# Optimization experiments

Hardware: AMD Instinct MI355X
Metric: run time of the kernel (lower is better)

Reference implementation:

```python
import jax, jax.numpy as jnp
import numpy as np

N = 100000        # nodes
E = 1600000       # edges
DES, TWEET, NUMP, CATP = 768, 768, 6, 11
IN_DIM, H, R = 512, 128, 2
BR = IN_DIM // 4  # per-branch width = 128


def setup_inputs() -> dict:
    key = jax.random.key(0)
    ks = jax.random.split(key, 16)
    w = lambda k, s: jax.random.normal(k, s, jnp.float32) * 0.02
    z = lambda d: jnp.zeros((d,), jnp.float32)
    return {
        "x": jax.random.normal(ks[0], (N, NUMP + TWEET + CATP + DES), jnp.float32),
        "edge_index": jax.random.randint(ks[1], (2, E), 0, N),
        "edge_type": jax.random.randint(ks[2], (E,), 0, R),
        "W_des": w(ks[3], (DES, BR)),   "b_des": z(BR),
        "W_tweet": w(ks[4], (TWEET, BR)), "b_tweet": z(BR),
        "W_num": w(ks[5], (NUMP, BR)),  "b_num": z(BR),
        "W_cat": w(ks[6], (CATP, BR)),  "b_cat": z(BR),
        "W_in": w(ks[7], (IN_DIM, H)),  "b_in": z(H),
        "prelu_a": jnp.full((H,), 0.25, jnp.float32),
        "root1": w(ks[8], (H, H)), "rel1": w(ks[9], (R, H, H)), "bias1": z(H),
        "root2": w(ks[10], (H, H)), "rel2": w(ks[11], (R, H, H)), "bias2": z(H),
        "W_cls": w(ks[12], (H, H)), "b_cls": z(H),
    }


def _leaky(v):
    return jnp.where(v >= 0, v, 0.01 * v)


def _rgcn(h, src, dst, edge_type, root, rel_w, bias):
    # PyG RGCNConv (default mean aggregation per relation):
    # out_i = bias + h_i @ root + sum_r mean_{j in N_r(i)} h_j @ W_r
    out = h @ root + bias
    for r in range(R):  # R is small and fixed
        mask = (edge_type == r).astype(h.dtype)          # [E]
        msg = (h @ rel_w[r])[src] * mask[:, None]        # [E, H]
        agg = jax.ops.segment_sum(msg, dst, num_segments=N)
        cnt = jax.ops.segment_sum(mask, dst, num_segments=N)
        out = out + agg / jnp.maximum(cnt, 1.0)[:, None]
    return out


def reference(x, edge_index, edge_type,
              W_des, b_des, W_tweet, b_tweet, W_num, b_num, W_cat, b_cat,
              W_in, b_in, prelu_a,
              root1, rel1, bias1, root2, rel2, bias2, W_cls, b_cls):
    # feature column layout: [num_prop | tweet | cat_prop | des]
    num_prop = x[:, :NUMP]
    tweet = x[:, NUMP:NUMP + TWEET]
    cat_prop = x[:, NUMP + TWEET:NUMP + TWEET + CATP]
    des = x[:, NUMP + TWEET + CATP:]

    d = _leaky(des @ W_des + b_des)
    t = _leaky(tweet @ W_tweet + b_tweet)
    n = _leaky(num_prop @ W_num + b_num)
    c = _leaky(cat_prop @ W_cat + b_cat)
    h = jnp.concatenate((d, t, n, c), axis=1) @ W_in + b_in
    h = jnp.where(h >= 0, h, prelu_a * h)  # PReLU, per-channel alpha

    src, dst = edge_index[0], edge_index[1]
    h = _rgcn(h, src, dst, edge_type, root1, rel1, bias1)
    h = _rgcn(h, src, dst, edge_type, root2, rel2, bias2)
    return h @ W_cls + b_cls
```

## Files before the change

kernel.cpp:

```cpp
#include <hip/hip_runtime.h>
#include <cstdint>
#include <cstddef>

#define NN 100000
#define EE 1600000
#define XDIM 1553
#define HD 128

typedef __attribute__((ext_vector_type(8))) short short8;
typedef __attribute__((ext_vector_type(4))) float f32x4;
typedef float f32x4u __attribute__((vector_size(16), aligned(4)));

union Frag { unsigned int u[4]; short8 s; uint4 v; };

#define OFF_DES_HI 0
#define OFF_DES_LO 98304
#define OFF_TW_HI  196608
#define OFF_TW_LO  294912
#define OFF_NUM_HI 393216
#define OFF_NUM_LO 397312
#define OFF_CAT_HI 401408
#define OFF_CAT_LO 405504
#define OFF_WIN_HI 409600
#define OFF_WIN_LO 475136
#define OFF_L1_HI  540672
#define OFF_L1_LO  589824
#define OFF_L2_HI  638976
#define OFF_L2_LO  688128
#define OFF_CLS_HI 737280
#define OFF_CLS_LO 753664
#define WT_SITES   385024

#define PREPW_BLOCKS 1504
#define COUNT_BLOCKS 6250
#define PROJ_NBLK    1563
#define FILL_BLOCKS  6250

__device__ __forceinline__ void cvt_pair(float f0, float f1,
                                         unsigned int& hi, unsigned int& lo) {
  unsigned int u0 = __float_as_uint(f0), u1 = __float_as_uint(f1);
  hi = __builtin_amdgcn_perm(u1, u0, 0x07060302u);
  float l0 = f0 - __uint_as_float(u0 & 0xFFFF0000u);
  float l1 = f1 - __uint_as_float(u1 & 0xFFFF0000u);
  lo = __builtin_amdgcn_perm(__float_as_uint(l1), __float_as_uint(l0), 0x07060302u);
}

__device__ __forceinline__ unsigned short bf16_rne(float f) {
  unsigned int u = __float_as_uint(f);
  return (unsigned short)((u + 0x7FFFu + ((u >> 16) & 1u)) >> 16);
}

__device__ __forceinline__ void fence_barrier() {
  asm volatile("" ::: "memory");
  __builtin_amdgcn_s_barrier();
  asm volatile("" ::: "memory");
}
__device__ __forceinline__ void lgkm0_barrier() {
  asm volatile("s_waitcnt lgkmcnt(0)" ::: "memory");
  __builtin_amdgcn_s_barrier();
  asm volatile("" ::: "memory");
}

__global__ __launch_bounds__(256) void k_setup(
    const float* __restrict__ Wdes, const float* __restrict__ Wtw,
    const float* __restrict__ Wnum, const float* __restrict__ Wcat,
    const float* __restrict__ Win,  const float* __restrict__ root1,
    const float* __restrict__ rel1, const float* __restrict__ root2,
    const float* __restrict__ rel2, const float* __restrict__ Wcls,
    unsigned short* __restrict__ Wt,
    const int* __restrict__ ei, const int* __restrict__ et,
    int* __restrict__ cnt2) {
  if (blockIdx.x >= PREPW_BLOCKS) {
    int e = (blockIdx.x - PREPW_BLOCKS) * 256 + threadIdx.x;
    if (e < EE) atomicAdd(&cnt2[et[e] * NN + ei[EE + e]], 1);
    return;
  }
  int id = blockIdx.x * 256 + threadIdx.x;
  if (id >= WT_SITES) return;
  const float* src; int K, Kpad, dhi, dlo, local;
  if (id < 98304)       { src=Wdes;        K=768; Kpad=768; dhi=OFF_DES_HI;       dlo=OFF_DES_LO;       local=id; }
  else if (id < 196608) { src=Wtw;         K=768; Kpad=768; dhi=OFF_TW_HI;        dlo=OFF_TW_LO;        local=id-98304; }
  else if (id < 200704) { src=Wnum;        K=6;   Kpad=32;  dhi=OFF_NUM_HI;       dlo=OFF_NUM_LO;       local=id-196608; }
  else if (id < 204800) { src=Wcat;        K=11;  Kpad=32;  dhi=OFF_CAT_HI;       dlo=OFF_CAT_LO;       local=id-200704; }
  else if (id < 270336) { src=Win;         K=512; Kpad=512; dhi=OFF_WIN_HI;       dlo=OFF_WIN_LO;       local=id-204800; }
  else if (id < 286720) { src=root1;       K=128; Kpad=128; dhi=OFF_L1_HI;        dlo=OFF_L1_LO;        local=id-270336; }
  else if (id < 303104) { src=rel1;        K=128; Kpad=128; dhi=OFF_L1_HI+16384;  dlo=OFF_L1_LO+16384;  local=id-286720; }
  else if (id < 319488) { src=rel1+16384;  K=128; Kpad=128; dhi=OFF_L1_HI+32768;  dlo=OFF_L1_LO+32768;  local=id-303104; }
  else if (id < 335872) { src=root2;       K=128; Kpad=128; dhi=OFF_L2_HI;        dlo=OFF_L2_LO;        local=id-319488; }
  else if (id < 352256) { src=rel2;        K=128; Kpad=128; dhi=OFF_L2_HI+16384;  dlo=OFF_L2_LO+16384;  local=id-335872; }
  else if (id < 368640) { src=rel2+16384;  K=128; Kpad=128; dhi=OFF_L2_HI+32768;  dlo=OFF_L2_LO+32768;  local=id-352256; }
  else                  { src=Wcls;        K=128; Kpad=128; dhi=OFF_CLS_HI;       dlo=OFF_CLS_LO;       local=id-368640; }
  int col = local / Kpad;
  int k = local - col * Kpad;
  float v = (k < K) ? src[(size_t)k * 128 + col] : 0.f;
  unsigned int u = __float_as_uint(v);
  float lo = v - __uint_as_float(u & 0xFFFF0000u);
  Wt[dhi + col * Kpad + k] = (unsigned short)(u >> 16);
  Wt[dlo + col * Kpad + k] = (unsigned short)(__float_as_uint(lo) >> 16);
}

__global__ __launch_bounds__(128) void k_fusew(
    const float* __restrict__ root2, const float* __restrict__ rel2,
    const float* __restrict__ Wcls,  const float* __restrict__ bias2,
    const float* __restrict__ bcls,  unsigned short* __restrict__ Wt,
    float* __restrict__ bfused) {
  int k = blockIdx.x;
  int c = threadIdx.x;
  const float* wrow;
  if (k < 128)      wrow = root2 + (size_t)k * 128;
  else if (k < 256) wrow = rel2 + (size_t)(k - 128) * 128;
  else if (k < 384) wrow = rel2 + 16384 + (size_t)(k - 256) * 128;
  else              wrow = bias2;
  float s = 0.f;
  for (int j = 0; j < 128; ++j) s += wrow[j] * Wcls[(size_t)j * 128 + c];
  if (k == 384) { bfused[c] = s + bcls[c]; return; }
  unsigned int u = __float_as_uint(s);
  float lo = s - __uint_as_float(u & 0xFFFF0000u);
  int sub = k >> 7, kl = k & 127;
  Wt[OFF_L2_HI + sub * 16384 + c * 128 + kl] = (unsigned short)(u >> 16);
  Wt[OFF_L2_LO + sub * 16384 + c * 128 + kl] = (unsigned short)(__float_as_uint(lo) >> 16);
}

__global__ __launch_bounds__(256) void k_scan1(const int* __restrict__ cnt2,
                                               int* __restrict__ row_ptr,
                                               int* __restrict__ bsum) {
  __shared__ int sums[256];
  int t = threadIdx.x;
  int base = blockIdx.x * 1024 + t * 4;
  int v[4]; int s = 0;
#pragma unroll
  for (int j = 0; j < 4; ++j) {
    int idx = base + j;
    v[j] = (idx < NN) ? (cnt2[idx] + cnt2[NN + idx]) : 0;
    s += v[j];
  }
  sums[t] = s;
  __syncthreads();
  for (int d = 1; d < 256; d <<= 1) {
    int val = (t >= d) ? sums[t - d] : 0;
    __syncthreads();
    sums[t] += val;
    __syncthreads();
  }
  int excl = sums[t] - s;
  if (t == 255) bsum[blockIdx.x] = sums[t];
  int run = excl;
#pragma unroll
  for (int j = 0; j < 4; ++j) {
    int idx = base + j;
    if (idx < NN) row_ptr[idx] = run;
    run += v[j];
  }
}

__global__ __launch_bounds__(128) void k_scan2(int* __restrict__ bsum, int nb) {
  __shared__ int s[128];
  int t = threadIdx.x;
  int v = (t < nb) ? bsum[t] : 0;
  s[t] = v;
  __syncthreads();
  for (int d = 1; d < 128; d <<= 1) {
    int val = (t >= d) ? s[t - d] : 0;
    __syncthreads();
    s[t] += val;
    __syncthreads();
  }
  if (t < nb) bsum[t] = s[t] - v;
}

__global__ __launch_bounds__(256) void k_scan3(int* __restrict__ row_ptr,
                                               const int* __restrict__ bsum) {
  int idx = blockIdx.x * 256 + threadIdx.x;
  if (idx < NN) row_ptr[idx] += bsum[idx >> 10];
  if (idx == NN) row_ptr[NN] = EE;
}

__global__ __launch_bounds__(256, 3) void k_proj2(
    const float* __restrict__ x,
    const float* __restrict__ bdes, const float* __restrict__ btw,
    const float* __restrict__ bnum, const float* __restrict__ bcat,
    const float* __restrict__ bin,  const float* __restrict__ pa,
    const unsigned short* __restrict__ Wt, float* __restrict__ h0,
    unsigned short* __restrict__ h16,
    const int* __restrict__ ei, const int* __restrict__ et,
    const int* __restrict__ row_ptr, int* __restrict__ fillpos,
    int* __restrict__ entries) {
  __shared__ unsigned short bt_hi[128 * 32], bt_lo[128 * 32];
  __shared__ unsigned short z_hi[64 * 128], z_lo[64 * 128];

  if (blockIdx.x >= PROJ_NBLK) {
    int e = (blockIdx.x - PROJ_NBLK) * 256 + threadIdx.x;
    if (e < EE) {
      int src = ei[e];
      int dst = ei[EE + e];
      int r = et[e];
      int pos = atomicAdd(&fillpos[dst], 1);
      entries[row_ptr[dst] + pos] = src | (r << 20);
    }
    return;
  }

  const int t = threadIdx.x;
  const int node0 = blockIdx.x * 64;
  const int w = t >> 6, lane = t & 63;
  const int li = lane & 15, lg = lane >> 4;

  const int cr0 = t >> 2, c0 = t & 3;
  const int cr1 = cr0 + 64;
  const unsigned stb0 = cr0 * 64 + ((c0 ^ ((cr0 >> 1) & 3)) << 4);
  const unsigned stb1 = cr1 * 64 + ((c0 ^ ((cr1 >> 1) & 3)) << 4);

  const int rowA = w * 16 + li;
  int nodeA = node0 + rowA;
  int ndA = nodeA < NN ? nodeA : NN - 1;
  const float* xrow = x + (size_t)ndA * XDIM;

#define STORE_BT(SH0, SL0, SH1, SL1)              \
  do {                                            \
    *(uint4*)((char*)bt_hi + stb0) = (SH0);       \
    *(uint4*)((char*)bt_lo + stb0) = (SL0);       \
    *(uint4*)((char*)bt_hi + stb1) = (SH1);       \
    *(uint4*)((char*)bt_lo + stb1) = (SL1);       \
  } while (0)

#define CVT_A2(FA, FB, AH, AL)                                                   \
  do {                                                                           \
    cvt_pair((FA)[0], (FA)[1], (AH).u[0], (AL).u[0]);                            \
    cvt_pair((FA)[2], (FA)[3], (AH).u[1], (AL).u[1]);                            \
    cvt_pair((FB)[0], (FB)[1], (AH).u[2], (AL).u[2]);                            \
    cvt_pair((FB)[2], (FB)[3], (AH).u[3], (AL).u[3]);                            \
  } while (0)

#define MFMA8(AH, AL, ACC)                                                       \
  do {                                                                           \
    _Pragma("unroll")                                                            \
    for (int ct_ = 0; ct_ < 8; ++ct_) {                                          \
      int colrow_ = ct_ * 16 + li;                                               \
      int byte_ = colrow_ * 64 + (lg << 4);                                      \
      byte_ ^= ((colrow_ >> 1) & 3) << 4;                                        \
      Frag bh_, bl_;                                                             \
      bh_.v = *(const uint4*)((char*)bt_hi + byte_);                             \
      bl_.v = *(const uint4*)((char*)bt_lo + byte_);                             \
      (ACC)[ct_] = __builtin_amdgcn_mfma_f32_16x16x32_bf16((AH).s, bl_.s, (ACC)[ct_], 0, 0, 0); \
      (ACC)[ct_] = __builtin_amdgcn_mfma_f32_16x16x32_bf16((AL).s, bh_.s, (ACC)[ct_], 0, 0, 0); \
      (ACC)[ct_] = __builtin_amdgcn_mfma_f32_16x16x32_bf16((AH).s, bh_.s, (ACC)[ct_], 0, 0, 0); \
    }                                                                            \
  } while (0)

#define TILE(WC0, WC1, WC2, WC3, WN0, WN1, WN2, WN3, XA, XB, T)                  \
  do {                                                                           \
    STORE_BT(WC0, WC1, WC2, WC3);                                                \
    lgkm0_barrier();                                                             \
    Frag ah_, al_;                                                               \
    CVT_A2(XA, XB, ah_, al_);                                                    \
    {                                                                            \
      const int kw_ = ((T) + 1) * 32;                                            \
      WN0 = *(const uint4*)(ph0 + kw_); WN1 = *(const uint4*)(pl0 + kw_);        \
      WN2 = *(const uint4*)(ph1 + kw_); WN3 = *(const uint4*)(pl1 + kw_);        \
      int kx_ = (T) + 3; if (kx_ > 23) kx_ = 23; kx_ *= 32;                      \
      XA = *(const f32x4u*)(xr + kx_);                                           \
      XB = *(const f32x4u*)(xr + kx_ + 4);                                       \
    }                                                                            \
    MFMA8(ah_, al_, zacc);                                                       \
    fence_barrier();                                                             \
  } while (0)

#define MFMA_B(KT)                                                               \
  do {                                                                           \
    Frag ah_, al_;                                                               \
    int byte_ = rowA * 256 + (((KT) * 32 + lg * 8) << 1);                        \
    byte_ ^= (rowA & 7) << 4;                                                    \
    ah_.v = *(const uint4*)((char*)z_hi + byte_);                                \
    al_.v = *(const uint4*)((char*)z_lo + byte_);                                \
    MFMA8(ah_, al_, hacc);                                                       \
  } while (0)

#define Z_EPI(ZACC, BIASP)                                                       \
  do {                                                                           \
    _Pragma("unroll")                                                            \
    for (int ct_ = 0; ct_ < 8; ++ct_) {                                          \
      int col_ = ct_ * 16 + li;                                                  \
      float bv_ = (BIASP)[col_];                                                 \
      _Pragma("unroll")                                                          \
      for (int r_ = 0; r_ < 4; ++r_) {                                           \
        float v_ = (ZACC)[ct_][r_] + bv_;                                        \
        v_ = v_ >= 0.f ? v_ : 0.01f * v_;                                        \
        int row_ = w * 16 + lg * 4 + r_;                                         \
        int byte_ = row_ * 256 + col_ * 2;                                       \
        byte_ ^= (row_ & 7) << 4;                                                \
        unsigned int u_ = __float_as_uint(v_);                                   \
        *(unsigned short*)((char*)z_hi + byte_) = (unsigned short)(u_ >> 16);    \
        float lo_ = v_ - __uint_as_float(u_ & 0xFFFF0000u);                      \
        *(unsigned short*)((char*)z_lo + byte_) = (unsigned short)(__float_as_uint(lo_) >> 16); \
      }                                                                          \
    }                                                                            \
  } while (0)

#define PHASE_B(SLICE)                                                           \
  do {                                                                           \
    const unsigned short* qh0_ = Wt + OFF_WIN_HI + cr0 * 512 + (SLICE) * 128 + c0 * 8; \
    const unsigned short* ql0_ = Wt + OFF_WIN_LO + cr0 * 512 + (SLICE) * 128 + c0 * 8; \
    const unsigned short* qh1_ = Wt + OFF_WIN_HI + cr1 * 512 + (SLICE) * 128 + c0 * 8; \
    const unsigned short* ql1_ = Wt + OFF_WIN_LO + cr1 * 512 + (SLICE) * 128 + c0 * 8; \
    uint4 wA0_ = *(const uint4*)(qh0_), wA1_ = *(const uint4*)(ql0_);            \
    uint4 wA2_ = *(const uint4*)(qh1_), wA3_ = *(const uint4*)(ql1_);            \
    uint4 wB0_, wB1_, wB2_, wB3_;                                                \
    STORE_BT(wA0_, wA1_, wA2_, wA3_);                                            \
    lgkm0_barrier();                                                             \
    wB0_ = *(const uint4*)(qh0_ + 32); wB1_ = *(const uint4*)(ql0_ + 32);        \
    wB2_ = *(const uint4*)(qh1_ + 32); wB3_ = *(const uint4*)(ql1_ + 32);        \
    MFMA_B(0);                                                                   \
    fence_barrier();                                                             \
    STORE_BT(wB0_, wB1_, wB2_, wB3_);                                            \
    lgkm0_barrier();                                                             \
    wA0_ = *(const uint4*)(qh0_ + 64); wA1_ = *(const uint4*)(ql0_ + 64);        \
    wA2_ = *(const uint4*)(qh1_ + 64); wA3_ = *(const uint4*)(ql1_ + 64);        \
    MFMA_B(1);                                                                   \
    fence_barrier();                                                             \
    STORE_BT(wA0_, wA1_, wA2_, wA3_);                                            \
    lgkm0_barrier();                                                             \
    wB0_ = *(const uint4*)(qh0_ + 96); wB1_ = *(const uint4*)(ql0_ + 96);        \
    wB2_ = *(const uint4*)(qh1_ + 96); wB3_ = *(const uint4*)(ql1_ + 96);        \
    MFMA_B(2);                                                                   \
    fence_barrier();                                                             \
    STORE_BT(wB0_, wB1_, wB2_, wB3_);                                            \
    lgkm0_barrier();                                                             \
    MFMA_B(3);                                                                   \
    fence_barrier();                                                             \
  } while (0)

  f32x4 hacc[8];
#pragma unroll
  for (int b = 0; b < 8; ++b) hacc[b] = (f32x4)0.f;

#pragma unroll
  for (int s = 0; s < 2; ++s) {
    const int off = (s == 0) ? 785 : 6;
    const unsigned short* wh = Wt + (s == 0 ? OFF_DES_HI : OFF_TW_HI);
    const unsigned short* wl = Wt + (s == 0 ? OFF_DES_LO : OFF_TW_LO);
    const float* bias = (s == 0) ? bdes : btw;

    const float* xr = xrow + off + lg * 8;
    const unsigned short* ph0 = wh + cr0 * 768 + c0 * 8;
    const unsigned short* pl0 = wl + cr0 * 768 + c0 * 8;
    const unsigned short* ph1 = wh + cr1 * 768 + c0 * 8;
    const unsigned short* pl1 = wl + cr1 * 768 + c0 * 8;

    f32x4 zacc[8];
#pragma unroll
    for (int b = 0; b < 8; ++b) zacc[b] = (f32x4)0.f;

    uint4 WA0, WA1, WA2, WA3, WB0, WB1, WB2, WB3;
    f32x4u X0a, X0b, X1a, X1b, X2a, X2b;

    WA0 = *(const uint4*)(ph0); WA1 = *(const uint4*)(pl0);
    WA2 = *(const uint4*)(ph1); WA3 = *(const uint4*)(pl1);
    X0a = *(const f32x4u*)(xr);      X0b = *(const f32x4u*)(xr + 4);
    X1a = *(const f32x4u*)(xr + 32); X1b = *(const f32x4u*)(xr + 36);
    X2a = *(const f32x4u*)(xr + 64); X2b = *(const f32x4u*)(xr + 68);

    for (int base = 0; base < 24; base += 6) {
      TILE(WA0, WA1, WA2, WA3, WB0, WB1, WB2, WB3, X0a, X0b, base + 0);
      TILE(WB0, WB1, WB2, WB3, WA0, WA1, WA2, WA3, X1a, X1b, base + 1);
      TILE(WA0, WA1, WA2, WA3, WB0, WB1, WB2, WB3, X2a, X2b, base + 2);
      TILE(WB0, WB1, WB2, WB3, WA0, WA1, WA2, WA3, X0a, X0b, base + 3);
      TILE(WA0, WA1, WA2, WA3, WB0, WB1, WB2, WB3, X1a, X1b, base + 4);
      TILE(WB0, WB1, WB2, WB3, WA0, WA1, WA2, WA3, X2a, X2b, base + 5);
    }
    Z_EPI(zacc, bias);
    PHASE_B(s);
  }

#pragma unroll
  for (int u = 0; u < 2; ++u) {
    const int offu = (u == 0) ? 0 : 774;
    const int Ksu = (u == 0) ? 6 : 11;
    const unsigned short* wh = Wt + (u == 0 ? OFF_NUM_HI : OFF_CAT_HI);
    const unsigned short* wl = Wt + (u == 0 ? OFF_NUM_LO : OFF_CAT_LO);
    const float* biasu = (u == 0) ? bnum : bcat;
    const float* xr = xrow + offu + lg * 8;

    uint4 s0 = *(const uint4*)(wh + cr0 * 32 + c0 * 8);
    uint4 s1 = *(const uint4*)(wl + cr0 * 32 + c0 * 8);
    uint4 s2 = *(const uint4*)(wh + cr1 * 32 + c0 * 8);
    uint4 s3 = *(const uint4*)(wl + cr1 * 32 + c0 * 8);
    f32x4u fa = *(const f32x4u*)(xr);
    f32x4u fb = *(const f32x4u*)(xr + 4);
#pragma unroll
    for (int j = 0; j < 4; ++j) {
      if (lg * 8 + j >= Ksu) fa[j] = 0.f;
      if (lg * 8 + 4 + j >= Ksu) fb[j] = 0.f;
    }

    f32x4 zacc[8];
#pragma unroll
    for (int b = 0; b < 8; ++b) zacc[b] = (f32x4)0.f;

    STORE_BT(s0, s1, s2, s3);
    lgkm0_barrier();
    {
      Frag ah_, al_;
      CVT_A2(fa, fb, ah_, al_);
      MFMA8(ah_, al_, zacc);
    }
    fence_barrier();
    Z_EPI(zacc, biasu);
    PHASE_B(u + 2);
  }

#pragma unroll
  for (int ct = 0; ct < 8; ++ct) {
    int col = ct * 16 + li;
    float bi = bin[col];
    float p = pa[col];
#pragma unroll
    for (int r = 0; r < 4; ++r) {
      int node = node0 + w * 16 + lg * 4 + r;
      if (node < NN) {
        float v = hacc[ct][r] + bi;
        v = v >= 0.f ? v : p * v;
        h0[(size_t)node * HD + col] = v;
        h16[(size_t)node * HD + col] = bf16_rne(v);
      }
    }
  }

#undef TILE
#undef MFMA_B
#undef Z_EPI
#undef PHASE_B
}

__global__ __launch_bounds__(256) void k_gather(
    const unsigned short* __restrict__ h16, float* __restrict__ aggH,
    const int* __restrict__ row_ptr, const int* __restrict__ cnt2,
    const int* __restrict__ entries) {
  int i = blockIdx.x * 4 + (threadIdx.x >> 6);
  int l = threadIdx.x & 63;
  if (i >= NN) return;
  int rs = row_ptr[i], re = row_ptr[i + 1];
  int c0 = cnt2[i], c1 = cnt2[NN + i];
  float inv0 = 1.f / (float)(c0 > 0 ? c0 : 1);
  float inv1 = 1.f / (float)(c1 > 0 ? c1 : 1);
  float a0 = 0, a1 = 0, b0 = 0, b1 = 0;
  int e = rs;
  for (; e + 3 < re; e += 4) {
    int ent0 = entries[e], ent1 = entries[e + 1];
    int ent2 = entries[e + 2], ent3 = entries[e + 3];
    unsigned int p0 = ((const unsigned int*)(h16 + (size_t)(ent0 & 0xFFFFF) * HD))[l];
    unsigned int p1 = ((const unsigned int*)(h16 + (size_t)(ent1 & 0xFFFFF) * HD))[l];
    unsigned int p2 = ((const unsigned int*)(h16 + (size_t)(ent2 & 0xFFFFF) * HD))[l];
    unsigned int p3 = ((const unsigned int*)(h16 + (size_t)(ent3 & 0xFFFFF) * HD))[l];
    float v0x = __uint_as_float(p0 << 16), v0y = __uint_as_float(p0 & 0xFFFF0000u);
    float v1x = __uint_as_float(p1 << 16), v1y = __uint_as_float(p1 & 0xFFFF0000u);
    float v2x = __uint_as_float(p2 << 16), v2y = __uint_as_float(p2 & 0xFFFF0000u);
    float v3x = __uint_as_float(p3 << 16), v3y = __uint_as_float(p3 & 0xFFFF0000u);
    if (ent0 >> 20) { b0 += v0x; b1 += v0y; } else { a0 += v0x; a1 += v0y; }
    if (ent1 >> 20) { b0 += v1x; b1 += v1y; } else { a0 += v1x; a1 += v1y; }
    if (ent2 >> 20) { b0 += v2x; b1 += v2y; } else { a0 += v2x; a1 += v2y; }
    if (ent3 >> 20) { b0 += v3x; b1 += v3y; } else { a0 += v3x; a1 += v3y; }
  }
  for (; e < re; ++e) {
    int ent = entries[e];
    unsigned int p0 = ((const unsigned int*)(h16 + (size_t)(ent & 0xFFFFF) * HD))[l];
    float v0x = __uint_as_float(p0 << 16), v0y = __uint_as_float(p0 & 0xFFFF0000u);
    if (ent >> 20) { b0 += v0x; b1 += v0y; } else { a0 += v0x; a1 += v0y; }
  }
  float2* p0w = (float2*)(aggH + (size_t)i * HD);
  float2* p1w = (float2*)(aggH + (size_t)NN * HD + (size_t)i * HD);
  p0w[l] = make_float2(a0 * inv0, a1 * inv0);
  p1w[l] = make_float2(b0 * inv1, b1 * inv1);
}

__global__ __launch_bounds__(256, 4) void k_rgemm2(
    const float* __restrict__ hin, const float* __restrict__ aggH,
    const unsigned short* __restrict__ wl_hi, const unsigned short* __restrict__ wl_lo,
    const float* __restrict__ bias, float* __restrict__ outp,
    unsigned short* __restrict__ h16out) {
  __shared__ unsigned short bt_hi[128 * 32], bt_lo[128 * 32];

  const int t = threadIdx.x;
  const int node0 = blockIdx.x * 64;
  const int w = t >> 6, lane = t & 63;
  const int li = lane & 15, lg = lane >> 4;

  const int cr0 = t >> 2, c0 = t & 3;
  const int cr1 = cr0 + 64;
  const unsigned stb0 = cr0 * 64 + ((c0 ^ ((cr0 >> 1) & 3)) << 4);
  const unsigned stb1 = cr1 * 64 + ((c0 ^ ((cr1 >> 1) & 3)) << 4);

  const int rowA = w * 16 + li;
  int nodeA = node0 + rowA;
  int ndA = nodeA < NN ? nodeA : NN - 1;
  const float* a0p = hin + (size_t)ndA * HD + lg * 8;
  const float* a1p = aggH + (size_t)ndA * HD + lg * 8;
  const float* a2p = aggH + (size_t)NN * HD + (size_t)ndA * HD + lg * 8;

#define W2H(KT, CR) (wl_hi + ((KT) >> 2) * 16384 + (CR) * 128 + ((KT) & 3) * 32 + c0 * 8)
#define W2L(KT, CR) (wl_lo + ((KT) >> 2) * 16384 + (CR) * 128 + ((KT) & 3) * 32 + c0 * 8)

#define TILE2(WC0, WC1, WC2, WC3, WN0, WN1, WN2, WN3, XA, XB, T)                 \
  do {                                                                           \
    STORE_BT(WC0, WC1, WC2, WC3);                                                \
    lgkm0_barrier();                                                             \
    Frag ah_, al_;                                                               \
    CVT_A2(XA, XB, ah_, al_);                                                    \
    {                                                                            \
      int kn_ = (T) + 1; if (kn_ > 11) kn_ = 11;                                 \
      WN0 = *(const uint4*)W2H(kn_, cr0); WN1 = *(const uint4*)W2L(kn_, cr0);    \
      WN2 = *(const uint4*)W2H(kn_, cr1); WN3 = *(const uint4*)W2L(kn_, cr1);    \
      int kx_ = (T) + 3; if (kx_ > 11) kx_ = 11;                                 \
      const float* ap_ = (kx_ < 4) ? a0p : (kx_ < 8) ? a1p : a2p;                \
      XA = *(const f32x4u*)(ap_ + (kx_ & 3) * 32);                               \
      XB = *(const f32x4u*)(ap_ + (kx_ & 3) * 32 + 4);                           \
    }                                                                            \
    MFMA8(ah_, al_, acc);                                                        \
    fence_barrier();                                                             \
  } while (0)

  f32x4 acc[8];
#pragma unroll
  for (int b = 0; b < 8; ++b) acc[b] = (f32x4)0.f;

  uint4 WA0, WA1, WA2, WA3, WB0, WB1, WB2, WB3;
  f32x4u X0a, X0b, X1a, X1b, X2a, X2b;

  WA0 = *(const uint4*)W2H(0, cr0); WA1 = *(const uint4*)W2L(0, cr0);
  WA2 = *(const uint4*)W2H(0, cr1); WA3 = *(const uint4*)W2L(0, cr1);
  X0a = *(const f32x4u*)(a0p);      X0b = *(const f32x4u*)(a0p + 4);
  X1a = *(const f32x4u*)(a0p + 32); X1b = *(const f32x4u*)(a0p + 36);
  X2a = *(const f32x4u*)(a0p + 64); X2b = *(const f32x4u*)(a0p + 68);

  TILE2(WA0, WA1, WA2, WA3, WB0, WB1, WB2, WB3, X0a, X0b, 0);
  TILE2(WB0, WB1, WB2, WB3, WA0, WA1, WA2, WA3, X1a, X1b, 1);
  TILE2(WA0, WA1, WA2, WA3, WB0, WB1, WB2, WB3, X2a, X2b, 2);
  TILE2(WB0, WB1, WB2, WB3, WA0, WA1, WA2, WA3, X0a, X0b, 3);
  TILE2(WA0, WA1, WA2, WA3, WB0, WB1, WB2, WB3, X1a, X1b, 4);
  TILE2(WB0, WB1, WB2, WB3, WA0, WA1, WA2, WA3, X2a, X2b, 5);
  TILE2(WA0, WA1, WA2, WA3, WB0, WB1, WB2, WB3, X0a, X0b, 6);
  TILE2(WB0, WB1, WB2, WB3, WA0, WA1, WA2, WA3, X1a, X1b, 7);
  TILE2(WA0, WA1, WA2, WA3, WB0, WB1, WB2, WB3, X2a, X2b, 8);
  TILE2(WB0, WB1, WB2, WB3, WA0, WA1, WA2, WA3, X0a, X0b, 9);
  TILE2(WA0, WA1, WA2, WA3, WB0, WB1, WB2, WB3, X1a, X1b, 10);
  TILE2(WB0, WB1, WB2, WB3, WA0, WA1, WA2, WA3, X2a, X2b, 11);

#pragma unroll
  for (int ct = 0; ct < 8; ++ct) {
    int col = ct * 16 + li;
    float bv = bias[col];
#pragma unroll
    for (int r = 0; r < 4; ++r) {
      int node = node0 + w * 16 + lg * 4 + r;
      if (node < NN) {
        float v = acc[ct][r] + bv;
        outp[(size_t)node * HD + col] = v;
        if (h16out) h16out[(size_t)node * HD + col] = bf16_rne(v);
      }
    }
  }

#undef W2H
#undef W2L
#undef TILE2
}

extern "C" void kernel_launch(void* const* d_in, const int* in_sizes, int n_in,
                              void* d_out, int out_size, void* d_ws, size_t ws_size,
                              hipStream_t stream) {
  const float* x    = (const float*)d_in[0];
  const int* ei     = (const int*)d_in[1];
  const int* et     = (const int*)d_in[2];
  const float* Wdes = (const float*)d_in[3];
  const float* bdes = (const float*)d_in[4];
  const float* Wtw  = (const float*)d_in[5];
  const float* btw  = (const float*)d_in[6];
  const float* Wnum = (const float*)d_in[7];
  const float* bnum = (const float*)d_in[8];
  const float* Wcat = (const float*)d_in[9];
  const float* bcat = (const float*)d_in[10];
  const float* Win  = (const float*)d_in[11];
  const float* bin  = (const float*)d_in[12];
  const float* pa   = (const float*)d_in[13];
  const float* root1 = (const float*)d_in[14];
  const float* rel1  = (const float*)d_in[15];
  const float* bias1 = (const float*)d_in[16];
  const float* root2 = (const float*)d_in[17];
  const float* rel2  = (const float*)d_in[18];
  const float* bias2 = (const float*)d_in[19];
  const float* Wcls  = (const float*)d_in[20];
  const float* bcls  = (const float*)d_in[21];
  float* out = (float*)d_out;

  char* p = (char*)d_ws;
  float* aggH = (float*)p;    p += (size_t)2 * NN * HD * 4;
  float* hB = (float*)p;      p += (size_t)NN * HD * 4;
  int* row_ptr = (int*)p;     p += ((size_t)NN + 4) * 4;
  int* cnt2 = (int*)p;        p += (size_t)2 * NN * 4;
  int* fillpos = (int*)p;     p += (size_t)NN * 4;
  int* entries = (int*)p;     p += (size_t)EE * 4;
  int* bsum = (int*)p;        p += 512;
  float* bfused = (float*)p;  p += 512;
  unsigned short* h16 = (unsigned short*)p; p += (size_t)NN * HD * 2;
  unsigned short* Wt = (unsigned short*)p;  p += (size_t)WT_SITES * 2 * 2;

  (void)hipMemsetAsync(cnt2, 0, (size_t)3 * NN * 4, stream);
  k_setup<<<PREPW_BLOCKS + COUNT_BLOCKS, 256, 0, stream>>>(
      Wdes, Wtw, Wnum, Wcat, Win, root1, rel1, root2, rel2, Wcls, Wt,
      ei, et, cnt2);
  k_fusew<<<385, 128, 0, stream>>>(root2, rel2, Wcls, bias2, bcls, Wt, bfused);

  int nb = (NN + 1023) / 1024;
  k_scan1<<<nb, 256, 0, stream>>>(cnt2, row_ptr, bsum);
  k_scan2<<<1, 128, 0, stream>>>(bsum, nb);
  k_scan3<<<(NN + 1 + 255) / 256, 256, 0, stream>>>(row_ptr, bsum);

  k_proj2<<<PROJ_NBLK + FILL_BLOCKS, 256, 0, stream>>>(
      x, bdes, btw, bnum, bcat, bin, pa, Wt, out, h16,
      ei, et, row_ptr, fillpos, entries);
  k_gather<<<NN / 4, 256, 0, stream>>>(h16, aggH, row_ptr, cnt2, entries);
  k_rgemm2<<<PROJ_NBLK, 256, 0, stream>>>(out, aggH, Wt + OFF_L1_HI, Wt + OFF_L1_LO,
                                          bias1, hB, h16);
  k_gather<<<NN / 4, 256, 0, stream>>>(h16, aggH, row_ptr, cnt2, entries);
  k_rgemm2<<<PROJ_NBLK, 256, 0, stream>>>(hB, aggH, Wt + OFF_L2_HI, Wt + OFF_L2_LO,
                                          bfused, out, (unsigned short*)nullptr);
}
```

Before: 867.0 us.

## Double node tile in input projection kernel to 128 rows per block

The fused input-projection kernel now processes 128 nodes per block instead of 64. Each wave computes two 16-row sub-tiles against every weight tile staged in LDS, which halves the weight staging and barrier traffic per node. In exchange the LDS intermediate buffer doubles, register pressure roughly doubles (occupancy hint drops from 3 to 2 blocks), the x prefetch depth shrinks from two tiles ahead to one, and the grid has fewer projection blocks. Helper macros are duplicated into the second GEMM kernel, which keeps its 64-row tiling.

```diff
diff --git a/kernel.cpp b/kernel.cpp
--- a/kernel.cpp
+++ b/kernel.cpp
@@ -33,7 +33,8 @@
 
 #define PREPW_BLOCKS 1504
 #define COUNT_BLOCKS 6250
-#define PROJ_NBLK    1563
+#define NBLK64       1563
+#define PROJ128_NBLK 782
 #define FILL_BLOCKS  6250
 
 __device__ __forceinline__ void cvt_pair(float f0, float f1,
@@ -175,7 +176,7 @@
   if (idx == NN) row_ptr[NN] = EE;
 }
 
-__global__ __launch_bounds__(256, 3) void k_proj2(
+__global__ __launch_bounds__(256, 2) void k_proj2(
     const float* __restrict__ x,
     const float* __restrict__ bdes, const float* __restrict__ btw,
     const float* __restrict__ bnum, const float* __restrict__ bcat,
@@ -186,10 +187,10 @@
     const int* __restrict__ row_ptr, int* __restrict__ fillpos,
     int* __restrict__ entries) {
   __shared__ unsigned short bt_hi[128 * 32], bt_lo[128 * 32];
-  __shared__ unsigned short z_hi[64 * 128], z_lo[64 * 128];
-
-  if (blockIdx.x >= PROJ_NBLK) {
-    int e = (blockIdx.x - PROJ_NBLK) * 256 + threadIdx.x;
+  __shared__ unsigned short z_hi[128 * 128], z_lo[128 * 128];
+
+  if (blockIdx.x >= PROJ128_NBLK) {
+    int e = (blockIdx.x - PROJ128_NBLK) * 256 + threadIdx.x;
     if (e < EE) {
       int src = ei[e];
       int dst = ei[EE + e];
@@ -201,7 +202,7 @@
   }
 
   const int t = threadIdx.x;
-  const int node0 = blockIdx.x * 64;
+  const int node0 = blockIdx.x * 128;
   const int w = t >> 6, lane = t & 63;
   const int li = lane & 15, lg = lane >> 4;
 
@@ -210,10 +211,12 @@
   const unsigned stb0 = cr0 * 64 + ((c0 ^ ((cr0 >> 1) & 3)) << 4);
   const unsigned stb1 = cr1 * 64 + ((c0 ^ ((cr1 >> 1) & 3)) << 4);
 
-  const int rowA = w * 16 + li;
-  int nodeA = node0 + rowA;
-  int ndA = nodeA < NN ? nodeA : NN - 1;
-  const float* xrow = x + (size_t)ndA * XDIM;
+  const int rowA0 = w * 32 + li;
+  const int rowA1 = rowA0 + 16;
+  int nodeA0 = node0 + rowA0; int nd0 = nodeA0 < NN ? nodeA0 : NN - 1;
+  int nodeA1 = node0 + rowA1; int nd1 = nodeA1 < NN ? nodeA1 : NN - 1;
+  const float* xrow0 = x + (size_t)nd0 * XDIM;
+  const float* xrow1 = x + (size_t)nd1 * XDIM;
 
 #define STORE_BT(SH0, SL0, SH1, SL1)              \
   do {                                            \
@@ -231,7 +234,7 @@
     cvt_pair((FB)[2], (FB)[3], (AH).u[3], (AL).u[3]);                            \
   } while (0)
 
-#define MFMA8(AH, AL, ACC)                                                       \
+#define MFMA8_2(A0H, A0L, A1H, A1L, ACC)                                         \
   do {                                                                           \
     _Pragma("unroll")                                                            \
     for (int ct_ = 0; ct_ < 8; ++ct_) {                                          \
@@ -241,38 +244,50 @@
       Frag bh_, bl_;                                                             \
       bh_.v = *(const uint4*)((char*)bt_hi + byte_);                             \
       bl_.v = *(const uint4*)((char*)bt_lo + byte_);                             \
-      (ACC)[ct_] = __builtin_amdgcn_mfma_f32_16x16x32_bf16((AH).s, bl_.s, (ACC)[ct_], 0, 0, 0); \
-      (ACC)[ct_] = __builtin_amdgcn_mfma_f32_16x16x32_bf16((AL).s, bh_.s, (ACC)[ct_], 0, 0, 0); \
-      (ACC)[ct_] = __builtin_amdgcn_mfma_f32_16x16x32_bf16((AH).s, bh_.s, (ACC)[ct_], 0, 0, 0); \
+      (ACC)[0][ct_] = __builtin_amdgcn_mfma_f32_16x16x32_bf16((A0H).s, bl_.s, (ACC)[0][ct_], 0, 0, 0); \
+      (ACC)[0][ct_] = __builtin_amdgcn_mfma_f32_16x16x32_bf16((A0L).s, bh_.s, (ACC)[0][ct_], 0, 0, 0); \
+      (ACC)[0][ct_] = __builtin_amdgcn_mfma_f32_16x16x32_bf16((A0H).s, bh_.s, (ACC)[0][ct_], 0, 0, 0); \
+      (ACC)[1][ct_] = __builtin_amdgcn_mfma_f32_16x16x32_bf16((A1H).s, bl_.s, (ACC)[1][ct_], 0, 0, 0); \
+      (ACC)[1][ct_] = __builtin_amdgcn_mfma_f32_16x16x32_bf16((A1L).s, bh_.s, (ACC)[1][ct_], 0, 0, 0); \
+      (ACC)[1][ct_] = __builtin_amdgcn_mfma_f32_16x16x32_bf16((A1H).s, bh_.s, (ACC)[1][ct_], 0, 0, 0); \
     }                                                                            \
   } while (0)
 
-#define TILE(WC0, WC1, WC2, WC3, WN0, WN1, WN2, WN3, XA, XB, T)                  \
+#define TILE(WC0, WC1, WC2, WC3, WN0, WN1, WN2, WN3, XA0, XB0, XA1, XB1, T)      \
   do {                                                                           \
     STORE_BT(WC0, WC1, WC2, WC3);                                                \
     lgkm0_barrier();                                                             \
-    Frag ah_, al_;                                                               \
-    CVT_A2(XA, XB, ah_, al_);                                                    \
+    Frag a0h_, a0l_, a1h_, a1l_;                                                 \
+    CVT_A2(XA0, XB0, a0h_, a0l_);                                                \
+    CVT_A2(XA1, XB1, a1h_, a1l_);                                                \
     {                                                                            \
       const int kw_ = ((T) + 1) * 32;                                            \
       WN0 = *(const uint4*)(ph0 + kw_); WN1 = *(const uint4*)(pl0 + kw_);        \
       WN2 = *(const uint4*)(ph1 + kw_); WN3 = *(const uint4*)(pl1 + kw_);        \
-      int kx_ = (T) + 3; if (kx_ > 23) kx_ = 23; kx_ *= 32;                      \
-      XA = *(const f32x4u*)(xr + kx_);                                           \
-      XB = *(const f32x4u*)(xr + kx_ + 4);                                       \
+      int kx_ = (T) + 2; if (kx_ > 23) kx_ = 23; kx_ *= 32;                      \
+      XA0 = *(const f32x4u*)(xr0 + kx_);                                         \
+      XB0 = *(const f32x4u*)(xr0 + kx_ + 4);                                     \
+      XA1 = *(const f32x4u*)(xr1 + kx_);                                         \
+      XB1 = *(const f32x4u*)(xr1 + kx_ + 4);                                     \
     }                                                                            \
-    MFMA8(ah_, al_, zacc);                                                       \
+    MFMA8_2(a0h_, a0l_, a1h_, a1l_, zacc);                                       \
     fence_barrier();                                                             \
   } while (0)
 
 #define MFMA_B(KT)                                                               \
   do {                                                                           \
-    Frag ah_, al_;                                                               \
-    int byte_ = rowA * 256 + (((KT) * 32 + lg * 8) << 1);                        \
-    byte_ ^= (rowA & 7) << 4;                                                    \
-    ah_.v = *(const uint4*)((char*)z_hi + byte_);                                \
-    al_.v = *(const uint4*)((char*)z_lo + byte_);                                \
-    MFMA8(ah_, al_, hacc);                                                       \
+    Frag a0h_, a0l_, a1h_, a1l_;                                                 \
+    {                                                                            \
+      int byte0_ = rowA0 * 256 + (((KT) * 32 + lg * 8) << 1);                    \
+      byte0_ ^= (rowA0 & 7) << 4;                                                \
+      a0h_.v = *(const uint4*)((char*)z_hi + byte0_);                            \
+      a0l_.v = *(const uint4*)((char*)z_lo + byte0_);                            \
+      int byte1_ = rowA1 * 256 + (((KT) * 32 + lg * 8) << 1);                    \
+      byte1_ ^= (rowA1 & 7) << 4;                                                \
+      a1h_.v = *(const uint4*)((char*)z_hi + byte1_);                            \
+      a1l_.v = *(const uint4*)((char*)z_lo + byte1_);                            \
+    }                                                                            \
+    MFMA8_2(a0h_, a0l_, a1h_, a1l_, hacc);                                       \
   } while (0)
 
 #define Z_EPI(ZACC, BIASP)                                                       \
@@ -282,16 +297,19 @@
       int col_ = ct_ * 16 + li;                                                  \
       float bv_ = (BIASP)[col_];                                                 \
       _Pragma("unroll")                                                          \
-      for (int r_ = 0; r_ < 4; ++r_) {                                           \
-        float v_ = (ZACC)[ct_][r_] + bv_;                                        \
-        v_ = v_ >= 0.f ? v_ : 0.01f * v_;                                        \
-        int row_ = w * 16 + lg * 4 + r_;                                         \
-        int byte_ = row_ * 256 + col_ * 2;                                       \
-        byte_ ^= (row_ & 7) << 4;                                                \
-        unsigned int u_ = __float_as_uint(v_);                                   \
-        *(unsigned short*)((char*)z_hi + byte_) = (unsigned short)(u_ >> 16);    \
-        float lo_ = v_ - __uint_as_float(u_ & 0xFFFF0000u);                      \
-        *(unsigned short*)((char*)z_lo + byte_) = (unsigned short)(__float_as_uint(lo_) >> 16); \
+      for (int sub_ = 0; sub_ < 2; ++sub_) {                                     \
+        _Pragma("unroll")                                                        \
+        for (int r_ = 0; r_ < 4; ++r_) {                                         \
+          float v_ = (ZACC)[sub_][ct_][r_] + bv_;                                \
+          v_ = v_ >= 0.f ? v_ : 0.01f * v_;                                      \
+          int row_ = w * 32 + sub_ * 16 + lg * 4 + r_;                           \
+          int byte_ = row_ * 256 + col_ * 2;                                     \
+          byte_ ^= (row_ & 7) << 4;                                              \
+          unsigned int u_ = __float_as_uint(v_);                                 \
+          *(unsigned short*)((char*)z_hi + byte_) = (unsigned short)(u_ >> 16);  \
+          float lo_ = v_ - __uint_as_float(u_ & 0xFFFF0000u);                    \
+          *(unsigned short*)((char*)z_lo + byte_) = (unsigned short)(__float_as_uint(lo_) >> 16); \
+        }                                                                        \
       }                                                                          \
     }                                                                            \
   } while (0)
@@ -329,9 +347,11 @@
     fence_barrier();                                                             \
   } while (0)
 
-  f32x4 hacc[8];
-#pragma unroll
-  for (int b = 0; b < 8; ++b) hacc[b] = (f32x4)0.f;
+  f32x4 hacc[2][8];
+#pragma unroll
+  for (int a = 0; a < 2; ++a)
+#pragma unroll
+    for (int b = 0; b < 8; ++b) hacc[a][b] = (f32x4)0.f;
 
 #pragma unroll
   for (int s = 0; s < 2; ++s) {
@@ -340,32 +360,32 @@
     const unsigned short* wl = Wt + (s == 0 ? OFF_DES_LO : OFF_TW_LO);
     const float* bias = (s == 0) ? bdes : btw;
 
-    const float* xr = xrow + off + lg * 8;
+    const float* xr0 = xrow0 + off + lg * 8;
+    const float* xr1 = xrow1 + off + lg * 8;
     const unsigned short* ph0 = wh + cr0 * 768 + c0 * 8;
     const unsigned short* pl0 = wl + cr0 * 768 + c0 * 8;
     const unsigned short* ph1 = wh + cr1 * 768 + c0 * 8;
     const unsigned short* pl1 = wl + cr1 * 768 + c0 * 8;
 
-    f32x4 zacc[8];
-#pragma unroll
-    for (int b = 0; b < 8; ++b) zacc[b] = (f32x4)0.f;
+    f32x4 zacc[2][8];
+#pragma unroll
+    for (int a = 0; a < 2; ++a)
+#pragma unroll
+      for (int b = 0; b < 8; ++b) zacc[a][b] = (f32x4)0.f;
 
     uint4 WA0, WA1, WA2, WA3, WB0, WB1, WB2, WB3;
-    f32x4u X0a, X0b, X1a, X1b, X2a, X2b;
+    f32x4u X0a0, X0b0, X0a1, X0b1, X1a0, X1b0, X1a1, X1b1;
 
     WA0 = *(const uint4*)(ph0); WA1 = *(const uint4*)(pl0);
     WA2 = *(const uint4*)(ph1); WA3 = *(const uint4*)(pl1);
-    X0a = *(const f32x4u*)(xr);      X0b = *(const f32x4u*)(xr + 4);
-    X1a = *(const f32x4u*)(xr + 32); X1b = *(const f32x4u*)(xr + 36);
-    X2a = *(const f32x4u*)(xr + 64); X2b = *(const f32x4u*)(xr + 68);
-
-    for (int base = 0; base < 24; base += 6) {
-      TILE(WA0, WA1, WA2, WA3, WB0, WB1, WB2, WB3, X0a, X0b, base + 0);
-      TILE(WB0, WB1, WB2, WB3, WA0, WA1, WA2, WA3, X1a, X1b, base + 1);
-      TILE(WA0, WA1, WA2, WA3, WB0, WB1, WB2, WB3, X2a, X2b, base + 2);
-      TILE(WB0, WB1, WB2, WB3, WA0, WA1, WA2, WA3, X0a, X0b, base + 3);
-      TILE(WA0, WA1, WA2, WA3, WB0, WB1, WB2, WB3, X1a, X1b, base + 4);
-      TILE(WB0, WB1, WB2, WB3, WA0, WA1, WA2, WA3, X2a, X2b, base + 5);
+    X0a0 = *(const f32x4u*)(xr0);      X0b0 = *(const f32x4u*)(xr0 + 4);
+    X0a1 = *(const f32x4u*)(xr1);      X0b1 = *(const f32x4u*)(xr1 + 4);
+    X1a0 = *(const f32x4u*)(xr0 + 32); X1b0 = *(const f32x4u*)(xr0 + 36);
+    X1a1 = *(const f32x4u*)(xr1 + 32); X1b1 = *(const f32x4u*)(xr1 + 36);
+
+    for (int base = 0; base < 24; base += 2) {
+      TILE(WA0, WA1, WA2, WA3, WB0, WB1, WB2, WB3, X0a0, X0b0, X0a1, X0b1, base + 0);
+      TILE(WB0, WB1, WB2, WB3, WA0, WA1, WA2, WA3, X1a0, X1b0, X1a1, X1b1, base + 1);
     }
     Z_EPI(zacc, bias);
     PHASE_B(s);
@@ -378,30 +398,36 @@
     const unsigned short* wh = Wt + (u == 0 ? OFF_NUM_HI : OFF_CAT_HI);
     const unsigned short* wl = Wt + (u == 0 ? OFF_NUM_LO : OFF_CAT_LO);
     const float* biasu = (u == 0) ? bnum : bcat;
-    const float* xr = xrow + offu + lg * 8;
+    const float* xr0 = xrow0 + offu + lg * 8;
+    const float* xr1 = xrow1 + offu + lg * 8;
 
     uint4 s0 = *(const uint4*)(wh + cr0 * 32 + c0 * 8);
     uint4 s1 = *(const uint4*)(wl + cr0 * 32 + c0 * 8);
     uint4 s2 = *(const uint4*)(wh + cr1 * 32 + c0 * 8);
     uint4 s3 = *(const uint4*)(wl + cr1 * 32 + c0 * 8);
-    f32x4u fa = *(const f32x4u*)(xr);
-    f32x4u fb = *(const f32x4u*)(xr + 4);
+    f32x4u fa0 = *(const f32x4u*)(xr0);
+    f32x4u fb0 = *(const f32x4u*)(xr0 + 4);
+    f32x4u fa1 = *(const f32x4u*)(xr1);
+    f32x4u fb1 = *(const f32x4u*)(xr1 + 4);
 #pragma unroll
     for (int j = 0; j < 4; ++j) {
-      if (lg * 8 + j >= Ksu) fa[j] = 0.f;
-      if (lg * 8 + 4 + j >= Ksu) fb[j] = 0.f;
+      if (lg * 8 + j >= Ksu) { fa0[j] = 0.f; fa1[j] = 0.f; }
+      if (lg * 8 + 4 + j >= Ksu) { fb0[j] = 0.f; fb1[j] = 0.f; }
     }
 
-    f32x4 zacc[8];
-#pragma unroll
-    for (int b = 0; b < 8; ++b) zacc[b] = (f32x4)0.f;
+    f32x4 zacc[2][8];
+#pragma unroll
+    for (int a = 0; a < 2; ++a)
+#pragma unroll
+      for (int b = 0; b < 8; ++b) zacc[a][b] = (f32x4)0.f;
 
     STORE_BT(s0, s1, s2, s3);
     lgkm0_barrier();
     {
-      Frag ah_, al_;
-      CVT_A2(fa, fb, ah_, al_);
-      MFMA8(ah_, al_, zacc);
+      Frag a0h_, a0l_, a1h_, a1l_;
+      CVT_A2(fa0, fb0, a0h_, a0l_);
+      CVT_A2(fa1, fb1, a1h_, a1l_);
+      MFMA8_2(a0h_, a0l_, a1h_, a1l_, zacc);
     }
     fence_barrier();
     Z_EPI(zacc, biasu);
@@ -414,13 +440,16 @@
     float bi = bin[col];
     float p = pa[col];
 #pragma unroll
-    for (int r = 0; r < 4; ++r) {
-      int node = node0 + w * 16 + lg * 4 + r;
-      if (node < NN) {
-        float v = hacc[ct][r] + bi;
-        v = v >= 0.f ? v : p * v;
-        h0[(size_t)node * HD + col] = v;
-        h16[(size_t)node * HD + col] = bf16_rne(v);
+    for (int sub = 0; sub < 2; ++sub) {
+#pragma unroll
+      for (int r = 0; r < 4; ++r) {
+        int node = node0 + w * 32 + sub * 16 + lg * 4 + r;
+        if (node < NN) {
+          float v = hacc[sub][ct][r] + bi;
+          v = v >= 0.f ? v : p * v;
+          h0[(size_t)node * HD + col] = v;
+          h16[(size_t)node * HD + col] = bf16_rne(v);
+        }
       }
     }
   }
@@ -429,6 +458,7 @@
 #undef MFMA_B
 #undef Z_EPI
 #undef PHASE_B
+#undef MFMA8_2
 }
 
 __global__ __launch_bounds__(256) void k_gather(
@@ -496,6 +526,38 @@
   const float* a1p = aggH + (size_t)ndA * HD + lg * 8;
   const float* a2p = aggH + (size_t)NN * HD + (size_t)ndA * HD + lg * 8;
 
+#define STORE_BT(SH0, SL0, SH1, SL1)              \
+  do {                                            \
+    *(uint4*)((char*)bt_hi + stb0) = (SH0);       \
+    *(uint4*)((char*)bt_lo + stb0) = (SL0);       \
+    *(uint4*)((char*)bt_hi + stb1) = (SH1);       \
+    *(uint4*)((char*)bt_lo + stb1) = (SL1);       \
+  } while (0)
+
+#define CVT_A2(FA, FB, AH, AL)                                                   \
+  do {                                                                           \
+    cvt_pair((FA)[0], (FA)[1], (AH).u[0], (AL).u[0]);                            \
+    cvt_pair((FA)[2], (FA)[3], (AH).u[1], (AL).u[1]);                            \
+    cvt_pair((FB)[0], (FB)[1], (AH).u[2], (AL).u[2]);                            \
+    cvt_pair((FB)[2], (FB)[3], (AH).u[3], (AL).u[3]);                            \
+  } while (0)
+
+#define MFMA8(AH, AL, ACC)                                                       \
+  do {                                                                           \
+    _Pragma("unroll")                                                            \
+    for (int ct_ = 0; ct_ < 8; ++ct_) {                                          \
+      int colrow_ = ct_ * 16 + li;                                               \
+      int byte_ = colrow_ * 64 + (lg << 4);                                      \
+      byte_ ^= ((colrow_ >> 1) & 3) << 4;                                        \
+      Frag bh_, bl_;                                                             \
+      bh_.v = *(const uint4*)((char*)bt_hi + byte_);                             \
+      bl_.v = *(const uint4*)((char*)bt_lo + byte_);                             \
+      (ACC)[ct_] = __builtin_amdgcn_mfma_f32_16x16x32_bf16((AH).s, bl_.s, (ACC)[ct_], 0, 0, 0); \
+      (ACC)[ct_] = __builtin_amdgcn_mfma_f32_16x16x32_bf16((AL).s, bh_.s, (ACC)[ct_], 0, 0, 0); \
+      (ACC)[ct_] = __builtin_amdgcn_mfma_f32_16x16x32_bf16((AH).s, bh_.s, (ACC)[ct_], 0, 0, 0); \
+    }                                                                            \
+  } while (0)
+
 #define W2H(KT, CR) (wl_hi + ((KT) >> 2) * 16384 + (CR) * 128 + ((KT) & 3) * 32 + c0 * 8)
 #define W2L(KT, CR) (wl_lo + ((KT) >> 2) * 16384 + (CR) * 128 + ((KT) & 3) * 32 + c0 * 8)
 
@@ -562,6 +624,9 @@
 #undef W2H
 #undef W2L
 #undef TILE2
+#undef MFMA8
+#undef CVT_A2
+#undef STORE_BT
 }
 
 extern "C" void kernel_launch(void* const* d_in, const int* in_sizes, int n_in,
@@ -614,13 +679,13 @@
   k_scan2<<<1, 128, 0, stream>>>(bsum, nb);
   k_scan3<<<(NN + 1 + 255) / 256, 256, 0, stream>>>(row_ptr, bsum);
 
-  k_proj2<<<PROJ_NBLK + FILL_BLOCKS, 256, 0, stream>>>(
+  k_proj2<<<PROJ128_NBLK + FILL_BLOCKS, 256, 0, stream>>>(
       x, bdes, btw, bnum, bcat, bin, pa, Wt, out, h16,
       ei, et, row_ptr, fillpos, entries);
   k_gather<<<NN / 4, 256, 0, stream>>>(h16, aggH, row_ptr, cnt2, entries);
-  k_rgemm2<<<PROJ_NBLK, 256, 0, stream>>>(out, aggH, Wt + OFF_L1_HI, Wt + OFF_L1_LO,
-                                          bias1, hB, h16);
+  k_rgemm2<<<NBLK64, 256, 0, stream>>>(out, aggH, Wt + OFF_L1_HI, Wt + OFF_L1_LO,
+                                       bias1, hB, h16);
   k_gather<<<NN / 4, 256, 0, stream>>>(h16, aggH, row_ptr, cnt2, entries);
-  k_rgemm2<<<PROJ_NBLK, 256, 0, stream>>>(hB, aggH, Wt + OFF_L2_HI, Wt + OFF_L2_LO,
-                                          bfused, out, (unsigned short*)nullptr);
-}
+  k_rgemm2<<<NBLK64, 256, 0, stream>>>(hB, aggH, Wt + OFF_L2_HI, Wt + OFF_L2_LO,
+                                       bfused, out, (unsigned short*)nullptr);
+}
```

After: 841.8 us. -2.9%, faster.
